# Kernel optimization log

Hardware: AMD Instinct MI355X
Metric: run time of the kernel (lower is better)

Reference implementation:

```python
import jax, jax.numpy as jnp
import numpy as np

B, T, HID = 2, 2048, 1536
H, HKV, D = 12, 2, 128
EPS = 1e-6
NEG = -1e9


def setup_inputs() -> dict:
    key = jax.random.key(0)
    ks = jax.random.split(key, 8)
    # rotary embeddings built from real angles (cos/sin of position*inv_freq)
    inv_freq = 1.0 / (10000.0 ** (jnp.arange(0, D, 2, dtype=jnp.float32) / D))  # [D/2]
    pos = jnp.arange(T, dtype=jnp.float32)
    ang = pos[:, None] * inv_freq[None, :]                       # [T, D/2]
    emb = jnp.concatenate([ang, ang], axis=-1)                   # [T, D]
    cos = jnp.broadcast_to(jnp.cos(emb)[None], (B, T, D))
    sin = jnp.broadcast_to(jnp.sin(emb)[None], (B, T, D))
    # additive causal mask [1,1,T,T]
    causal = jnp.tril(jnp.ones((T, T), dtype=bool))
    attention_mask = jnp.where(causal, 0.0, NEG).astype(jnp.float32)[None, None]
    s = 0.02
    return {
        "hidden_states": jax.random.normal(ks[0], (B, T, HID), jnp.float32),
        "cos": cos,
        "sin": sin,
        "attention_mask": attention_mask,
        "q_w": jax.random.normal(ks[1], (H * D, HID), jnp.float32) * s,
        "k_w": jax.random.normal(ks[2], (HKV * D, HID), jnp.float32) * s,
        "v_w": jax.random.normal(ks[3], (HKV * D, HID), jnp.float32) * s,
        "o_w": jax.random.normal(ks[4], (HID, H * D), jnp.float32) * s,
        "q_norm_w": jnp.ones((D,), jnp.float32),
        "k_norm_w": jnp.ones((D,), jnp.float32),
    }


def _rms_norm(x, w):
    # per-head RMSNorm over last dim (head_dim), computed in fp32
    xf = x.astype(jnp.float32)
    var = jnp.mean(xf * xf, axis=-1, keepdims=True)
    return (w * (xf * jax.lax.rsqrt(var + EPS))).astype(x.dtype)


def _rotate_half(x):
    x1, x2 = jnp.split(x, 2, axis=-1)
    return jnp.concatenate([-x2, x1], axis=-1)


def reference(hidden_states, cos, sin, attention_mask, q_w, k_w, v_w, o_w, q_norm_w, k_norm_w):
    b, t, _ = hidden_states.shape
    n_rep = H // HKV
    scale = D ** -0.5

    # projections -> [B, n_heads, T, D]
    q = (hidden_states @ q_w.T).reshape(b, t, H, D)
    k = (hidden_states @ k_w.T).reshape(b, t, HKV, D)
    v = (hidden_states @ v_w.T).reshape(b, t, HKV, D).transpose(0, 2, 1, 3)

    # per-head QK RMSNorm, then to [B, H, T, D]
    q = _rms_norm(q, q_norm_w).transpose(0, 2, 1, 3)
    k = _rms_norm(k, k_norm_w).transpose(0, 2, 1, 3)

    # RoPE (cos/sin broadcast over head axis)
    c = cos[:, None, :, :]
    s = sin[:, None, :, :]
    q = q * c + _rotate_half(q) * s
    k = k * c + _rotate_half(k) * s

    # GQA repeat_kv: [B, HKV, T, D] -> [B, H, T, D]
    k = jnp.repeat(k, n_rep, axis=1)
    v = jnp.repeat(v, n_rep, axis=1)

    attn = jnp.einsum('bhqd,bhkd->bhqk', q, k) * scale + attention_mask
    attn = jax.nn.softmax(attn.astype(jnp.float32), axis=-1).astype(q.dtype)
    out = jnp.einsum('bhqk,bhkd->bhqd', attn, v)
    out = out.transpose(0, 2, 1, 3).reshape(b, t, H * D)
    return out @ o_w.T
```

## Files before the change

### kernel.cpp

```cpp
#include <hip/hip_runtime.h>
#include <hip/hip_bf16.h>


#define B_   2
#define T_   2048
#define HID_ 1536
#define H_   12
#define HKV_ 2
#define D_   128
#define GQ_  (H_ / HKV_)
#define NQKV_ 2048
#define SCALE_ 0.08838834764831845f

typedef unsigned short u16;
typedef __attribute__((ext_vector_type(4))) float f32x4;
typedef __attribute__((ext_vector_type(8))) short bf16x8;
typedef __attribute__((ext_vector_type(4))) unsigned short u16x4;
typedef __attribute__((ext_vector_type(8))) unsigned short u16x8;

__device__ __forceinline__ u16 f2b(float f) {
  union { __hip_bfloat16 h; u16 u; } cv;
  cv.h = __float2bfloat16(f);
  return cv.u;
}
__device__ __forceinline__ float b2f(u16 u) {
  union { float f; unsigned i; } cv;
  cv.i = ((unsigned)u) << 16;
  return cv.f;
}

__device__ __forceinline__ void glds16(const u16* g, u16* l) {
  __builtin_amdgcn_global_load_lds((const __attribute__((address_space(1))) void*)g,
                                   (__attribute__((address_space(3))) void*)l, 16, 0, 0);
}

__global__ __launch_bounds__(256) void cvt_f32_bf16(const float* __restrict__ src,
                                                    u16* __restrict__ dst, int n4) {
  int i = blockIdx.x * 256 + threadIdx.x;
  const int stride = gridDim.x * 256;
  for (; i < n4; i += stride) {
    const float4 v = reinterpret_cast<const float4*>(src)[i];
    u16x4 o = {f2b(v.x), f2b(v.y), f2b(v.z), f2b(v.w)};
    reinterpret_cast<u16x4*>(dst)[i] = o;
  }
}

__device__ __forceinline__ void cstore(float* p, float v) { *p = v; }
__device__ __forceinline__ void cstore(u16* p, float v) { *p = f2b(v); }

template <typename CT>
__global__ __launch_bounds__(256) void gemm_bt(const u16* __restrict__ A,
                                               const u16* __restrict__ W,
                                               CT* __restrict__ C,
                                               int M, int N, int K) {
  __shared__ __align__(16) u16 As[128 * 32];
  __shared__ __align__(16) u16 Ws[128 * 32];
  const int tid  = threadIdx.x;
  const int lane = tid & 63;
  const int wid  = tid >> 6;
  const int wr = wid >> 1, wc = wid & 1;
  const int l15 = lane & 15, kg = lane >> 4;
  const int rowBase = blockIdx.y * 128;
  const int colBase = blockIdx.x * 128;

  const int srow = lane >> 2;
  const int scol = (lane & 3) << 3;
  const u16* Ab = A + (size_t)(rowBase + wid * 16 + srow) * K + scol;
  const u16* Wb = W + (size_t)(colBase + wid * 16 + srow) * K + scol;
  u16* AsW = &As[wid * 512];
  u16* WsW = &Ws[wid * 512];

  const f32x4 zero4 = {0.f, 0.f, 0.f, 0.f};
  f32x4 acc[4][4];
#pragma unroll
  for (int m = 0; m < 4; ++m)
#pragma unroll
    for (int n = 0; n < 4; ++n) acc[m][n] = zero4;

  for (int k0 = 0; k0 < K; k0 += 32) {
    __syncthreads();
    glds16(Ab + k0, AsW);
    glds16(Ab + (size_t)64 * K + k0, AsW + 2048);
    glds16(Wb + k0, WsW);
    glds16(Wb + (size_t)64 * K + k0, WsW + 2048);
    __syncthreads();
    bf16x8 a[4], b[4];
#pragma unroll
    for (int m = 0; m < 4; ++m)
      a[m] = *reinterpret_cast<const bf16x8*>(&As[(wr * 64 + m * 16 + l15) * 32 + kg * 8]);
#pragma unroll
    for (int n = 0; n < 4; ++n)
      b[n] = *reinterpret_cast<const bf16x8*>(&Ws[(wc * 64 + n * 16 + l15) * 32 + kg * 8]);
#pragma unroll
    for (int m = 0; m < 4; ++m)
#pragma unroll
      for (int n = 0; n < 4; ++n)
        acc[m][n] = __builtin_amdgcn_mfma_f32_16x16x32_bf16(a[m], b[n], acc[m][n], 0, 0, 0);
  }
#pragma unroll
  for (int m = 0; m < 4; ++m) {
    const int row0 = rowBase + wr * 64 + m * 16 + kg * 4;
#pragma unroll
    for (int n = 0; n < 4; ++n) {
      const int col = colBase + wc * 64 + n * 16 + l15;
#pragma unroll
      for (int r = 0; r < 4; ++r) cstore(&C[(size_t)(row0 + r) * N + col], acc[m][n][r]);
    }
  }
}

__global__ __launch_bounds__(256) void norm_rope_cvt(
    const u16* __restrict__ qkv, const float* __restrict__ cosb,
    const float* __restrict__ sinb, const float* __restrict__ q_nw,
    const float* __restrict__ k_nw, u16* __restrict__ q_b,
    u16* __restrict__ k_b, u16* __restrict__ vt_b) {
  const int gwave = (int)((blockIdx.x * 256 + threadIdx.x) >> 6);
  const int lane = threadIdx.x & 63;
  const int NQ = B_ * T_ * H_;
  const int NK = B_ * T_ * HKV_;
  if (gwave < NQ) {
    const int bt = gwave / H_, h = gwave - bt * H_;
    const u16* src = qkv + (size_t)bt * NQKV_ + h * D_;
    const float x1 = b2f(src[lane]), x2 = b2f(src[lane + 64]);
    float ss = x1 * x1 + x2 * x2;
#pragma unroll
    for (int m = 32; m >= 1; m >>= 1) ss += __shfl_xor(ss, m);
    const float rinv = rsqrtf(ss * (1.0f / D_) + 1e-6f);
    const float c1 = cosb[(size_t)bt * D_ + lane], c2 = cosb[(size_t)bt * D_ + lane + 64];
    const float s1 = sinb[(size_t)bt * D_ + lane], s2 = sinb[(size_t)bt * D_ + lane + 64];
    const float n1 = x1 * rinv * q_nw[lane], n2 = x2 * rinv * q_nw[lane + 64];
    const float o1 = (n1 * c1 - n2 * s1) * SCALE_;
    const float o2 = (n2 * c2 + n1 * s2) * SCALE_;
    const int b = bt >> 11, t = bt & (T_ - 1);
    u16* dst = q_b + ((size_t)(b * H_ + h) * T_ + t) * D_;
    dst[lane] = f2b(o1);
    dst[lane + 64] = f2b(o2);
  } else if (gwave < NQ + NK) {
    const int r = gwave - NQ;
    const int bt = r >> 1, hv = r & 1;
    const u16* src = qkv + (size_t)bt * NQKV_ + 1536 + hv * D_;
    const float x1 = b2f(src[lane]), x2 = b2f(src[lane + 64]);
    float ss = x1 * x1 + x2 * x2;
#pragma unroll
    for (int m = 32; m >= 1; m >>= 1) ss += __shfl_xor(ss, m);
    const float rinv = rsqrtf(ss * (1.0f / D_) + 1e-6f);
    const float c1 = cosb[(size_t)bt * D_ + lane], c2 = cosb[(size_t)bt * D_ + lane + 64];
    const float s1 = sinb[(size_t)bt * D_ + lane], s2 = sinb[(size_t)bt * D_ + lane + 64];
    const float n1 = x1 * rinv * k_nw[lane], n2 = x2 * rinv * k_nw[lane + 64];
    const float o1 = n1 * c1 - n2 * s1;
    const float o2 = n2 * c2 + n1 * s2;
    const int b = bt >> 11, t = bt & (T_ - 1);
    u16* dst = k_b + ((size_t)(b * HKV_ + hv) * T_ + t) * D_;
    dst[lane] = f2b(o1);
    dst[lane + 64] = f2b(o2);
  } else {
    const int r = gwave - NQ - NK;
    const int bt = r >> 1, hv = r & 1;
    const u16* src = qkv + (size_t)bt * NQKV_ + 1792 + hv * D_;
    const float x1 = b2f(src[lane]), x2 = b2f(src[lane + 64]);
    const int b = bt >> 11, t = bt & (T_ - 1);
    const int kk = t & 63;
    const int tp = (t & ~63) | (kk & 32) | (((kk >> 2) & 3) << 3) |
                   (((kk >> 4) & 1) << 2) | (kk & 3);
    u16* dst = vt_b + (size_t)(b * HKV_ + hv) * D_ * T_;
    dst[(size_t)lane * T_ + tp] = f2b(x1);
    dst[(size_t)(lane + 64) * T_ + tp] = f2b(x2);
  }
}

__constant__ int QT_ARR[40] = {15,15,15,15,14,14,11,11,11,10, 7, 7, 3,
                               14,14,13,13,13,13,12,12,10,10, 9, 9, 6, 6,
                               12,12, 9, 8, 8, 8, 5, 5, 2,
                                4, 4, 1, 0};
__constant__ int C_ARR[40]  = { 0, 1, 2, 3, 0, 1, 0, 1, 2, 0, 0, 1,-1,
                                2, 3, 0, 1, 2, 3, 0, 1, 1, 2, 0, 1, 0, 1,
                                2, 3, 2, 0, 1, 2, 0, 1,-1,
                                0, 1,-1,-1};
__device__ __forceinline__ int nc_of(int qt) { return (qt < 8) ? 2 : ((qt < 12) ? 3 : 4); }
__device__ __forceinline__ int mlbase_of(int qt) {
  return (qt < 8) ? 2 * (qt - 4) : ((qt < 12) ? 8 + 3 * (qt - 8) : 20 + 4 * (qt - 12));
}
__device__ __forceinline__ int pbase_of(int qt) {
  return (qt < 8) ? (qt - 4) : ((qt < 12) ? 4 + 2 * (qt - 8) : 12 + 3 * (qt - 12));
}

__global__ __launch_bounds__(256) void attn_kernel(const u16* __restrict__ q_b,
                                                   const u16* __restrict__ k_b,
                                                   const u16* __restrict__ vt_b,
                                                   u16* __restrict__ aout,
                                                   u16* __restrict__ po0,
                                                   float2* __restrict__ ml) {
  __shared__ __align__(16) u16 Ks[64 * 128];
  __shared__ __align__(16) u16 Vs[128 * 64];
  const int id = blockIdx.x;
  const int item = id / 24;
  const int bh = id - item * 24;
  const int qt = QT_ARR[item];
  const int c = C_ARR[item];
  int kt0, ktend;
  bool partial;
  if (c < 0) {
    kt0 = 0; ktend = 2 * qt + 1; partial = false;
  } else {
    const int nt = 2 * qt + 2;
    const int nc = nc_of(qt);
    const int base = nt / nc, rem = nt - base * nc;
    kt0 = c * base + (c < rem ? c : rem);
    ktend = kt0 + base + (c < rem ? 1 : 0) - 1;
    partial = true;
  }
  const int b = bh / H_, h = bh - b * H_;
  const int kvh = h / GQ_;
  const int tid = threadIdx.x;
  const int w = tid >> 6, lane = tid & 63;
  const int l15 = lane & 15, kg = lane >> 4;
  const int qbase = qt * 128;

  const u16* Kb = k_b + (size_t)(b * HKV_ + kvh) * T_ * D_;
  const u16* Vb = vt_b + (size_t)(b * HKV_ + kvh) * D_ * T_;

  bf16x8 qf[2][4];
#pragma unroll
  for (int qb = 0; qb < 2; ++qb) {
    const u16* qrow =
        q_b + ((size_t)(b * H_ + h) * T_ + qbase + w * 32 + qb * 16 + l15) * D_;
#pragma unroll
    for (int s4 = 0; s4 < 4; ++s4)
      qf[qb][s4] = *reinterpret_cast<const bf16x8*>(qrow + s4 * 32 + kg * 8);
  }

  int kK[4], vK[4];
#pragma unroll
  for (int cc = 0; cc < 4; ++cc) {
    const int ch = w * 4 + cc;
    const int kr = ch * 4 + (lane >> 4);
    kK[cc] = kr * D_ + (((lane & 15) << 3) ^ ((kr & 7) << 3));
    const int dr = ch * 8 + (lane >> 3);
    vK[cc] = dr * T_ + (((lane & 7) << 3) ^ ((dr & 7) << 3));
  }

  const int xorv = (l15 & 7) << 3;

  const f32x4 zero4 = {0.f, 0.f, 0.f, 0.f};
  f32x4 o[2][8];
#pragma unroll
  for (int qb = 0; qb < 2; ++qb)
#pragma unroll
    for (int n = 0; n < 8; ++n) o[qb][n] = zero4;
  float m[2] = {0.f, 0.f};
  float lsum[2] = {0.f, 0.f};

  for (int kt = kt0; kt <= ktend; ++kt) {
    __syncthreads();
    {
      const size_t kb = (size_t)kt * 64;
#pragma unroll
      for (int cc = 0; cc < 4; ++cc) {
        glds16(Kb + kb * D_ + kK[cc], &Ks[(w * 4 + cc) * 512]);
        glds16(Vb + kb + vK[cc], &Vs[(w * 4 + cc) * 512]);
      }
    }
    __syncthreads();
    f32x4 sc[2][4];
#pragma unroll
    for (int qb = 0; qb < 2; ++qb)
#pragma unroll
      for (int n = 0; n < 4; ++n) sc[qb][n] = zero4;
    __builtin_amdgcn_s_setprio(1);
#pragma unroll
    for (int n = 0; n < 4; ++n)
#pragma unroll
      for (int s4 = 0; s4 < 4; ++s4) {
        const int koff = (n * 16 + l15) * 128 + ((s4 * 32 + kg * 8) ^ xorv);
        bf16x8 kf = *reinterpret_cast<const bf16x8*>(&Ks[koff]);
#pragma unroll
        for (int qb = 0; qb < 2; ++qb)
          sc[qb][n] = __builtin_amdgcn_mfma_f32_16x16x32_bf16(kf, qf[qb][s4],
                                                              sc[qb][n], 0, 0, 0);
      }
    __builtin_amdgcn_s_setprio(0);
    if (kt >= 2 * qt) {
#pragma unroll
      for (int qb = 0; qb < 2; ++qb) {
        const int qg = w * 32 + qb * 16 + l15;
        const int kbb = (kt - 2 * qt) * 64;
#pragma unroll
        for (int n = 0; n < 4; ++n)
#pragma unroll
          for (int r = 0; r < 4; ++r)
            if (kbb + n * 16 + kg * 4 + r > qg) sc[qb][n][r] = -3e38f;
      }
    }
    float pm[2];
#pragma unroll
    for (int qb = 0; qb < 2; ++qb) {
      float v = sc[qb][0][0];
#pragma unroll
      for (int n = 0; n < 4; ++n)
#pragma unroll
        for (int r = 0; r < 4; ++r) v = fmaxf(v, sc[qb][n][r]);
      v = fmaxf(v, __shfl_xor(v, 16));
      v = fmaxf(v, __shfl_xor(v, 32));
      pm[qb] = v;
    }
    if (__any((pm[0] > m[0] + 8.f) | (pm[1] > m[1] + 8.f))) {
#pragma unroll
      for (int qb = 0; qb < 2; ++qb) {
        const float mn = fmaxf(m[qb], pm[qb]);
        const float al = __expf(m[qb] - mn);
        m[qb] = mn;
        lsum[qb] *= al;
        float alT[4];
#pragma unroll
        for (int r = 0; r < 4; ++r)
          alT[r] = __shfl(al, (lane & 48) | (kg * 4 + r));
#pragma unroll
        for (int n = 0; n < 8; ++n)
#pragma unroll
          for (int r = 0; r < 4; ++r) o[qb][n][r] *= alT[r];
      }
    }
#pragma unroll
    for (int qb = 0; qb < 2; ++qb) {
      float rs = 0.f;
#pragma unroll
      for (int n = 0; n < 4; ++n)
#pragma unroll
        for (int r = 0; r < 4; ++r) {
          const float p = __expf(sc[qb][n][r] - m[qb]);
          sc[qb][n][r] = p;
          rs += p;
        }
      rs += __shfl_xor(rs, 16);
      rs += __shfl_xor(rs, 32);
      lsum[qb] += rs;
    }
    bf16x8 pf[2][2];
#pragma unroll
    for (int qb = 0; qb < 2; ++qb)
#pragma unroll
      for (int ks = 0; ks < 2; ++ks)
#pragma unroll
        for (int r = 0; r < 4; ++r) {
          pf[qb][ks][r] = (short)f2b(sc[qb][2 * ks][r]);
          pf[qb][ks][r + 4] = (short)f2b(sc[qb][2 * ks + 1][r]);
        }
    __builtin_amdgcn_s_setprio(1);
#pragma unroll
    for (int n = 0; n < 8; ++n)
#pragma unroll
      for (int ks = 0; ks < 2; ++ks) {
        const int voff = (n * 16 + l15) * 64 + ((ks * 32 + kg * 8) ^ xorv);
        bf16x8 vf = *reinterpret_cast<const bf16x8*>(&Vs[voff]);
#pragma unroll
        for (int qb = 0; qb < 2; ++qb)
          o[qb][n] = __builtin_amdgcn_mfma_f32_16x16x32_bf16(pf[qb][ks], vf,
                                                             o[qb][n], 0, 0, 0);
      }
    __builtin_amdgcn_s_setprio(0);
  }

  if (!partial) {
    float invT[2][4];
#pragma unroll
    for (int qb = 0; qb < 2; ++qb) {
      const float inv = 1.0f / lsum[qb];
#pragma unroll
      for (int r = 0; r < 4; ++r)
        invT[qb][r] = __shfl(inv, (lane & 48) | (kg * 4 + r));
    }
#pragma unroll
    for (int qb = 0; qb < 2; ++qb) {
      const int t0 = qbase + w * 32 + qb * 16 + kg * 4;
#pragma unroll
      for (int n = 0; n < 8; ++n)
#pragma unroll
        for (int r = 0; r < 4; ++r)
          aout[(size_t)(b * T_ + t0 + r) * (H_ * D_) + h * D_ + n * 16 + l15] =
              f2b(o[qb][n][r] * invT[qb][r]);
    }
  } else {
    const int mlslot = bh * 36 + mlbase_of(qt) + c;
    if (kg == 0) {
#pragma unroll
      for (int qb = 0; qb < 2; ++qb) {
        float2 v;
        v.x = m[qb];
        v.y = lsum[qb];
        ml[(size_t)mlslot * 128 + w * 32 + qb * 16 + l15] = v;
      }
    }
    if (c == 0) {
#pragma unroll
      for (int qb = 0; qb < 2; ++qb) {
        const int t0 = qbase + w * 32 + qb * 16 + kg * 4;
#pragma unroll
        for (int n = 0; n < 8; ++n)
#pragma unroll
          for (int r = 0; r < 4; ++r)
            aout[(size_t)(b * T_ + t0 + r) * (H_ * D_) + h * D_ + n * 16 + l15] =
                f2b(o[qb][n][r]);
      }
    } else {
      const int pslot = bh * 24 + pbase_of(qt) + (c - 1);
#pragma unroll
      for (int qb = 0; qb < 2; ++qb) {
        const int row0 = w * 32 + qb * 16 + kg * 4;
#pragma unroll
        for (int n = 0; n < 8; ++n)
#pragma unroll
          for (int r = 0; r < 4; ++r)
            po0[((size_t)pslot * 128 + row0 + r) * 128 + n * 16 + l15] =
                f2b(o[qb][n][r]);
      }
    }
  }
}

__global__ __launch_bounds__(256) void combine_kernel(u16* __restrict__ aout,
                                                      const u16* __restrict__ po0,
                                                      const float2* __restrict__ ml) {
  const int qt = 4 + blockIdx.x;
  const int bh = blockIdx.y;
  const int nc = nc_of(qt);
  const int mlb = bh * 36 + mlbase_of(qt);
  const int pb = bh * 24 + pbase_of(qt);
  const int b = bh / H_, h = bh - b * H_;
  const int t0 = qt * 128;
  const int tid = threadIdx.x;
  const int row = tid >> 1;
  const int colc = (tid & 1) << 6;

  float ms[4], ls[4];
  float mm = -3e38f;
  for (int cc = 0; cc < nc; ++cc) {
    const float2 v = ml[(size_t)(mlb + cc) * 128 + row];
    ms[cc] = v.x; ls[cc] = v.y;
    mm = fmaxf(mm, v.x);
  }
  float lt = 0.f;
  float scl[4];
  for (int cc = 0; cc < nc; ++cc) {
    scl[cc] = __expf(ms[cc] - mm);
    lt += ls[cc] * scl[cc];
  }
  const float inv = 1.0f / lt;
  for (int cc = 0; cc < nc; ++cc) scl[cc] *= inv;

  u16* a = aout + (size_t)(b * T_ + t0 + row) * (H_ * D_) + h * D_ + colc;
#pragma unroll
  for (int j = 0; j < 8; ++j) {
    u16x8 v0 = *reinterpret_cast<const u16x8*>(a + j * 8);
    float acc[8];
#pragma unroll
    for (int e = 0; e < 8; ++e) acc[e] = b2f(v0[e]) * scl[0];
    for (int cc = 1; cc < nc; ++cc) {
      const u16* p = po0 + ((size_t)(pb + cc - 1) * 128 + row) * 128 + colc;
      u16x8 vc = *reinterpret_cast<const u16x8*>(p + j * 8);
#pragma unroll
      for (int e = 0; e < 8; ++e) acc[e] += b2f(vc[e]) * scl[cc];
    }
    u16x8 outv;
#pragma unroll
    for (int e = 0; e < 8; ++e) outv[e] = f2b(acc[e]);
    *reinterpret_cast<u16x8*>(a + j * 8) = outv;
  }
}

extern "C" void kernel_launch(void* const* d_in, const int* in_sizes, int n_in,
                              void* d_out, int out_size, void* d_ws, size_t ws_size,
                              hipStream_t stream) {
  const float* hidden = (const float*)d_in[0];
  const float* cosb   = (const float*)d_in[1];
  const float* sinb   = (const float*)d_in[2];
  const float* q_w  = (const float*)d_in[4];
  const float* k_w  = (const float*)d_in[5];
  const float* v_w  = (const float*)d_in[6];
  const float* o_w  = (const float*)d_in[7];
  const float* q_nw = (const float*)d_in[8];
  const float* k_nw = (const float*)d_in[9];
  float* out = (float*)d_out;

  char* ws = (char*)d_ws;
  const size_t MB = 1u << 20;
  u16*    hidden_b = (u16*)(ws);
  u16*    qkvw     = (u16*)(ws + 12 * MB);
  u16*    q_b      = (u16*)(ws);
  u16*    aout     = (u16*)(ws + 12 * MB);
  float2* ml       = (float2*)(ws + 24 * MB);
  u16*    k_b      = (u16*)(ws + 25 * MB);
  u16*    vt_b     = (u16*)(ws + 27 * MB);
  u16*    owb      = (u16*)(ws + 29 * MB);
  u16*    qkv_proj = (u16*)d_out;
  u16*    po0      = (u16*)d_out;

  const dim3 blk(256);
  const int M = B_ * T_;

  {
    const int nh = (B_ * T_ * HID_) / 4;
    const int nq = (H_ * D_ * HID_) / 4;
    const int nk = (HKV_ * D_ * HID_) / 4;
    cvt_f32_bf16<<<2048, blk, 0, stream>>>(hidden, hidden_b, nh);
    cvt_f32_bf16<<<2048, blk, 0, stream>>>(q_w, qkvw, nq);
    cvt_f32_bf16<<<384, blk, 0, stream>>>(k_w, qkvw + (size_t)1536 * HID_, nk);
    cvt_f32_bf16<<<384, blk, 0, stream>>>(v_w, qkvw + (size_t)1792 * HID_, nk);
    cvt_f32_bf16<<<2048, blk, 0, stream>>>(o_w, owb, nq);
  }

  gemm_bt<u16><<<dim3(NQKV_ / 128, M / 128), blk, 0, stream>>>(hidden_b, qkvw, qkv_proj,
                                                               M, NQKV_, HID_);

  norm_rope_cvt<<<16384, blk, 0, stream>>>(qkv_proj, cosb, sinb, q_nw, k_nw,
                                           q_b, k_b, vt_b);

  attn_kernel<<<960, blk, 0, stream>>>(q_b, k_b, vt_b, aout, po0, ml);
  combine_kernel<<<dim3(12, B_ * H_), blk, 0, stream>>>(aout, po0, ml);

  gemm_bt<float><<<dim3(HID_ / 128, M / 128), blk, 0, stream>>>(aout, owb, out,
                                                                M, HID_, HID_);
}
```

Before: 211.0 us.

## Fuse QK norm, RoPE and V transpose into QKV GEMM epilogue; use exp2 softmax

The QKV projection GEMM now stages its output tile in shared memory and applies per-head RMSNorm, RoPE and scaling directly in the epilogue, writing q/k/vt in the attention layout. This removes the separate norm_rope kernel and the round trip of the intermediate qkv buffer through global memory. The GEMM K-step is widened from 32 to 64, the three weight conversions are merged into one launch, and the log2(e) factor is folded into the Q scale so the softmax uses exp2f. The cost is a larger shared-memory footprint and a serial per-row epilogue loop within each block.

```diff
diff --git a/kernel.cpp b/kernel.cpp
--- a/kernel.cpp
+++ b/kernel.cpp
@@ -10,7 +10,8 @@
 #define D_   128
 #define GQ_  (H_ / HKV_)
 #define NQKV_ 2048
-#define SCALE_ 0.08838834764831845f
+#define LOG2E_ 1.4426950408889634f
+#define SCALE2_ (0.08838834764831845f * LOG2E_)
 
 typedef unsigned short u16;
 typedef __attribute__((ext_vector_type(4))) float f32x4;
@@ -45,16 +46,31 @@
   }
 }
 
-__device__ __forceinline__ void cstore(float* p, float v) { *p = v; }
-__device__ __forceinline__ void cstore(u16* p, float v) { *p = f2b(v); }
-
-template <typename CT>
+#define NQ4_ 589824
+#define NK4_ 98304
+__global__ __launch_bounds__(256) void cvt_wqkv(const float* __restrict__ q_w,
+                                                const float* __restrict__ k_w,
+                                                const float* __restrict__ v_w,
+                                                u16* __restrict__ qkvw) {
+  int i = blockIdx.x * 256 + threadIdx.x;
+  const int stride = gridDim.x * 256;
+  const int total = NQ4_ + 2 * NK4_;
+  for (; i < total; i += stride) {
+    float4 v;
+    if (i < NQ4_) v = reinterpret_cast<const float4*>(q_w)[i];
+    else if (i < NQ4_ + NK4_) v = reinterpret_cast<const float4*>(k_w)[i - NQ4_];
+    else v = reinterpret_cast<const float4*>(v_w)[i - NQ4_ - NK4_];
+    u16x4 o = {f2b(v.x), f2b(v.y), f2b(v.z), f2b(v.w)};
+    reinterpret_cast<u16x4*>(qkvw)[i] = o;
+  }
+}
+
 __global__ __launch_bounds__(256) void gemm_bt(const u16* __restrict__ A,
                                                const u16* __restrict__ W,
-                                               CT* __restrict__ C,
+                                               float* __restrict__ C,
                                                int M, int N, int K) {
-  __shared__ __align__(16) u16 As[128 * 32];
-  __shared__ __align__(16) u16 Ws[128 * 32];
+  __shared__ __align__(16) u16 As[128 * 64];
+  __shared__ __align__(16) u16 Ws[128 * 64];
   const int tid  = threadIdx.x;
   const int lane = tid & 63;
   const int wid  = tid >> 6;
@@ -63,12 +79,10 @@
   const int rowBase = blockIdx.y * 128;
   const int colBase = blockIdx.x * 128;
 
-  const int srow = lane >> 2;
-  const int scol = (lane & 3) << 3;
-  const u16* Ab = A + (size_t)(rowBase + wid * 16 + srow) * K + scol;
-  const u16* Wb = W + (size_t)(colBase + wid * 16 + srow) * K + scol;
-  u16* AsW = &As[wid * 512];
-  u16* WsW = &Ws[wid * 512];
+  const int srow = lane >> 3;
+  const int scol = (lane & 7) << 3;
+  const u16* Ab = A + (size_t)(rowBase + wid * 32 + srow) * K + scol;
+  const u16* Wb = W + (size_t)(colBase + wid * 32 + srow) * K + scol;
 
   const f32x4 zero4 = {0.f, 0.f, 0.f, 0.f};
   f32x4 acc[4][4];
@@ -77,25 +91,35 @@
 #pragma unroll
     for (int n = 0; n < 4; ++n) acc[m][n] = zero4;
 
-  for (int k0 = 0; k0 < K; k0 += 32) {
+  for (int k0 = 0; k0 < K; k0 += 64) {
     __syncthreads();
-    glds16(Ab + k0, AsW);
-    glds16(Ab + (size_t)64 * K + k0, AsW + 2048);
-    glds16(Wb + k0, WsW);
-    glds16(Wb + (size_t)64 * K + k0, WsW + 2048);
+#pragma unroll
+    for (int c = 0; c < 4; ++c) {
+      glds16(Ab + (size_t)(c * 8) * K + k0, &As[(wid * 4 + c) * 512]);
+      glds16(Wb + (size_t)(c * 8) * K + k0, &Ws[(wid * 4 + c) * 512]);
+    }
     __syncthreads();
-    bf16x8 a[4], b[4];
+    bf16x8 a[4][2], b[4][2];
 #pragma unroll
     for (int m = 0; m < 4; ++m)
-      a[m] = *reinterpret_cast<const bf16x8*>(&As[(wr * 64 + m * 16 + l15) * 32 + kg * 8]);
+#pragma unroll
+      for (int ks = 0; ks < 2; ++ks)
+        a[m][ks] = *reinterpret_cast<const bf16x8*>(
+            &As[(wr * 64 + m * 16 + l15) * 64 + ks * 32 + kg * 8]);
 #pragma unroll
     for (int n = 0; n < 4; ++n)
-      b[n] = *reinterpret_cast<const bf16x8*>(&Ws[(wc * 64 + n * 16 + l15) * 32 + kg * 8]);
+#pragma unroll
+      for (int ks = 0; ks < 2; ++ks)
+        b[n][ks] = *reinterpret_cast<const bf16x8*>(
+            &Ws[(wc * 64 + n * 16 + l15) * 64 + ks * 32 + kg * 8]);
 #pragma unroll
     for (int m = 0; m < 4; ++m)
 #pragma unroll
       for (int n = 0; n < 4; ++n)
-        acc[m][n] = __builtin_amdgcn_mfma_f32_16x16x32_bf16(a[m], b[n], acc[m][n], 0, 0, 0);
+#pragma unroll
+        for (int ks = 0; ks < 2; ++ks)
+          acc[m][n] = __builtin_amdgcn_mfma_f32_16x16x32_bf16(a[m][ks], b[n][ks],
+                                                              acc[m][n], 0, 0, 0);
   }
 #pragma unroll
   for (int m = 0; m < 4; ++m) {
@@ -104,67 +128,120 @@
     for (int n = 0; n < 4; ++n) {
       const int col = colBase + wc * 64 + n * 16 + l15;
 #pragma unroll
-      for (int r = 0; r < 4; ++r) cstore(&C[(size_t)(row0 + r) * N + col], acc[m][n][r]);
-    }
-  }
-}
-
-__global__ __launch_bounds__(256) void norm_rope_cvt(
-    const u16* __restrict__ qkv, const float* __restrict__ cosb,
-    const float* __restrict__ sinb, const float* __restrict__ q_nw,
-    const float* __restrict__ k_nw, u16* __restrict__ q_b,
-    u16* __restrict__ k_b, u16* __restrict__ vt_b) {
-  const int gwave = (int)((blockIdx.x * 256 + threadIdx.x) >> 6);
-  const int lane = threadIdx.x & 63;
-  const int NQ = B_ * T_ * H_;
-  const int NK = B_ * T_ * HKV_;
-  if (gwave < NQ) {
-    const int bt = gwave / H_, h = gwave - bt * H_;
-    const u16* src = qkv + (size_t)bt * NQKV_ + h * D_;
-    const float x1 = b2f(src[lane]), x2 = b2f(src[lane + 64]);
-    float ss = x1 * x1 + x2 * x2;
-#pragma unroll
-    for (int m = 32; m >= 1; m >>= 1) ss += __shfl_xor(ss, m);
-    const float rinv = rsqrtf(ss * (1.0f / D_) + 1e-6f);
-    const float c1 = cosb[(size_t)bt * D_ + lane], c2 = cosb[(size_t)bt * D_ + lane + 64];
-    const float s1 = sinb[(size_t)bt * D_ + lane], s2 = sinb[(size_t)bt * D_ + lane + 64];
-    const float n1 = x1 * rinv * q_nw[lane], n2 = x2 * rinv * q_nw[lane + 64];
-    const float o1 = (n1 * c1 - n2 * s1) * SCALE_;
-    const float o2 = (n2 * c2 + n1 * s2) * SCALE_;
-    const int b = bt >> 11, t = bt & (T_ - 1);
-    u16* dst = q_b + ((size_t)(b * H_ + h) * T_ + t) * D_;
-    dst[lane] = f2b(o1);
-    dst[lane + 64] = f2b(o2);
-  } else if (gwave < NQ + NK) {
-    const int r = gwave - NQ;
-    const int bt = r >> 1, hv = r & 1;
-    const u16* src = qkv + (size_t)bt * NQKV_ + 1536 + hv * D_;
-    const float x1 = b2f(src[lane]), x2 = b2f(src[lane + 64]);
-    float ss = x1 * x1 + x2 * x2;
-#pragma unroll
-    for (int m = 32; m >= 1; m >>= 1) ss += __shfl_xor(ss, m);
-    const float rinv = rsqrtf(ss * (1.0f / D_) + 1e-6f);
-    const float c1 = cosb[(size_t)bt * D_ + lane], c2 = cosb[(size_t)bt * D_ + lane + 64];
-    const float s1 = sinb[(size_t)bt * D_ + lane], s2 = sinb[(size_t)bt * D_ + lane + 64];
-    const float n1 = x1 * rinv * k_nw[lane], n2 = x2 * rinv * k_nw[lane + 64];
-    const float o1 = n1 * c1 - n2 * s1;
-    const float o2 = n2 * c2 + n1 * s2;
-    const int b = bt >> 11, t = bt & (T_ - 1);
-    u16* dst = k_b + ((size_t)(b * HKV_ + hv) * T_ + t) * D_;
-    dst[lane] = f2b(o1);
-    dst[lane + 64] = f2b(o2);
+      for (int r = 0; r < 4; ++r) C[(size_t)(row0 + r) * N + col] = acc[m][n][r];
+    }
+  }
+}
+
+__global__ __launch_bounds__(256) void gemm_qkv(
+    const u16* __restrict__ A, const u16* __restrict__ W,
+    const float* __restrict__ cosb, const float* __restrict__ sinb,
+    const float* __restrict__ q_nw, const float* __restrict__ k_nw,
+    u16* __restrict__ q_b, u16* __restrict__ k_b, u16* __restrict__ vt_b) {
+  __shared__ __align__(16) u16 smem[128 * 137];
+  u16* As = smem;
+  u16* Ws = smem + 8192;
+  const int tid  = threadIdx.x;
+  const int lane = tid & 63;
+  const int wid  = tid >> 6;
+  const int wr = wid >> 1, wc = wid & 1;
+  const int l15 = lane & 15, kg = lane >> 4;
+  const int rowBase = blockIdx.y * 128;
+  const int colBase = blockIdx.x * 128;
+  const int K = HID_;
+
+  const int srow = lane >> 3;
+  const int scol = (lane & 7) << 3;
+  const u16* Ab = A + (size_t)(rowBase + wid * 32 + srow) * K + scol;
+  const u16* Wb = W + (size_t)(colBase + wid * 32 + srow) * K + scol;
+
+  const f32x4 zero4 = {0.f, 0.f, 0.f, 0.f};
+  f32x4 acc[4][4];
+#pragma unroll
+  for (int m = 0; m < 4; ++m)
+#pragma unroll
+    for (int n = 0; n < 4; ++n) acc[m][n] = zero4;
+
+  for (int k0 = 0; k0 < K; k0 += 64) {
+    __syncthreads();
+#pragma unroll
+    for (int c = 0; c < 4; ++c) {
+      glds16(Ab + (size_t)(c * 8) * K + k0, &As[(wid * 4 + c) * 512]);
+      glds16(Wb + (size_t)(c * 8) * K + k0, &Ws[(wid * 4 + c) * 512]);
+    }
+    __syncthreads();
+    bf16x8 a[4][2], b[4][2];
+#pragma unroll
+    for (int m = 0; m < 4; ++m)
+#pragma unroll
+      for (int ks = 0; ks < 2; ++ks)
+        a[m][ks] = *reinterpret_cast<const bf16x8*>(
+            &As[(wr * 64 + m * 16 + l15) * 64 + ks * 32 + kg * 8]);
+#pragma unroll
+    for (int n = 0; n < 4; ++n)
+#pragma unroll
+      for (int ks = 0; ks < 2; ++ks)
+        b[n][ks] = *reinterpret_cast<const bf16x8*>(
+            &Ws[(wc * 64 + n * 16 + l15) * 64 + ks * 32 + kg * 8]);
+#pragma unroll
+    for (int m = 0; m < 4; ++m)
+#pragma unroll
+      for (int n = 0; n < 4; ++n)
+#pragma unroll
+        for (int ks = 0; ks < 2; ++ks)
+          acc[m][n] = __builtin_amdgcn_mfma_f32_16x16x32_bf16(a[m][ks], b[n][ks],
+                                                              acc[m][n], 0, 0, 0);
+  }
+
+  __syncthreads();
+#pragma unroll
+  for (int m = 0; m < 4; ++m)
+#pragma unroll
+    for (int n = 0; n < 4; ++n)
+#pragma unroll
+      for (int r = 0; r < 4; ++r)
+        smem[(wr * 64 + m * 16 + kg * 4 + r) * 137 + wc * 64 + n * 16 + l15] =
+            f2b(acc[m][n][r]);
+  __syncthreads();
+
+  const int ct = blockIdx.x;
+  const int b = rowBase >> 11;
+  if (ct < 14) {
+    const float* nw = (ct < 12) ? q_nw : k_nw;
+    const float nwl = nw[lane], nwh = nw[lane + 64];
+    const float sc = (ct < 12) ? SCALE2_ : 1.0f;
+    u16* dstbase = (ct < 12) ? (q_b + (size_t)(b * H_ + ct) * T_ * D_)
+                             : (k_b + (size_t)(b * HKV_ + (ct - 12)) * T_ * D_);
+    for (int i = 0; i < 32; ++i) {
+      const int row = wid * 32 + i;
+      const int tok = rowBase + row;
+      const int t = tok & (T_ - 1);
+      const float x1 = b2f(smem[row * 137 + lane]);
+      const float x2 = b2f(smem[row * 137 + lane + 64]);
+      float ss = x1 * x1 + x2 * x2;
+#pragma unroll
+      for (int msk = 32; msk >= 1; msk >>= 1) ss += __shfl_xor(ss, msk);
+      const float rinv = rsqrtf(ss * (1.0f / D_) + 1e-6f);
+      const float c1 = cosb[(size_t)tok * D_ + lane];
+      const float c2 = cosb[(size_t)tok * D_ + lane + 64];
+      const float s1 = sinb[(size_t)tok * D_ + lane];
+      const float s2 = sinb[(size_t)tok * D_ + lane + 64];
+      const float n1 = x1 * rinv * nwl, n2 = x2 * rinv * nwh;
+      u16* dst = dstbase + (size_t)t * D_;
+      dst[lane] = f2b((n1 * c1 - n2 * s1) * sc);
+      dst[lane + 64] = f2b((n2 * c2 + n1 * s2) * sc);
+    }
   } else {
-    const int r = gwave - NQ - NK;
-    const int bt = r >> 1, hv = r & 1;
-    const u16* src = qkv + (size_t)bt * NQKV_ + 1792 + hv * D_;
-    const float x1 = b2f(src[lane]), x2 = b2f(src[lane + 64]);
-    const int b = bt >> 11, t = bt & (T_ - 1);
-    const int kk = t & 63;
-    const int tp = (t & ~63) | (kk & 32) | (((kk >> 2) & 3) << 3) |
-                   (((kk >> 4) & 1) << 2) | (kk & 3);
-    u16* dst = vt_b + (size_t)(b * HKV_ + hv) * D_ * T_;
-    dst[(size_t)lane * T_ + tp] = f2b(x1);
-    dst[(size_t)(lane + 64) * T_ + tp] = f2b(x2);
+    const int hv = ct - 14;
+    const int tp = (lane & 32) | (((lane >> 2) & 3) << 3) | (((lane >> 4) & 1) << 2) |
+                   (lane & 3);
+    u16* vb = vt_b + (size_t)(b * HKV_ + hv) * D_ * T_;
+    const int tb = rowBase & (T_ - 1);
+    for (int it = 0; it < 64; ++it) {
+      const int d = wid * 32 + (it >> 1), half = it & 1;
+      const float x = b2f(smem[(half * 64 + lane) * 137 + d]);
+      vb[(size_t)d * T_ + tb + half * 64 + tp] = f2b(x);
+    }
   }
 }
 
@@ -238,7 +315,6 @@
     const int dr = ch * 8 + (lane >> 3);
     vK[cc] = dr * T_ + (((lane & 7) << 3) ^ ((dr & 7) << 3));
   }
-
   const int xorv = (l15 & 7) << 3;
 
   const f32x4 zero4 = {0.f, 0.f, 0.f, 0.f};
@@ -307,7 +383,7 @@
 #pragma unroll
       for (int qb = 0; qb < 2; ++qb) {
         const float mn = fmaxf(m[qb], pm[qb]);
-        const float al = __expf(m[qb] - mn);
+        const float al = exp2f(m[qb] - mn);
         m[qb] = mn;
         lsum[qb] *= al;
         float alT[4];
@@ -327,7 +403,7 @@
       for (int n = 0; n < 4; ++n)
 #pragma unroll
         for (int r = 0; r < 4; ++r) {
-          const float p = __expf(sc[qb][n][r] - m[qb]);
+          const float p = exp2f(sc[qb][n][r] - m[qb]);
           sc[qb][n][r] = p;
           rs += p;
         }
@@ -441,7 +517,7 @@
   float lt = 0.f;
   float scl[4];
   for (int cc = 0; cc < nc; ++cc) {
-    scl[cc] = __expf(ms[cc] - mm);
+    scl[cc] = exp2f(ms[cc] - mm);
     lt += ls[cc] * scl[cc];
   }
   const float inv = 1.0f / lt;
@@ -485,38 +561,28 @@
   const size_t MB = 1u << 20;
   u16*    hidden_b = (u16*)(ws);
   u16*    qkvw     = (u16*)(ws + 12 * MB);
-  u16*    q_b      = (u16*)(ws);
-  u16*    aout     = (u16*)(ws + 12 * MB);
-  float2* ml       = (float2*)(ws + 24 * MB);
-  u16*    k_b      = (u16*)(ws + 25 * MB);
-  u16*    vt_b     = (u16*)(ws + 27 * MB);
-  u16*    owb      = (u16*)(ws + 29 * MB);
-  u16*    qkv_proj = (u16*)d_out;
+  u16*    q_b      = (u16*)(ws + 18 * MB);
+  u16*    k_b      = (u16*)(ws + 30 * MB);
+  u16*    vt_b     = (u16*)(ws + 32 * MB);
+  u16*    aout     = (u16*)(ws);
+  u16*    owb      = (u16*)(ws + 12 * MB);
+  float2* ml       = (float2*)(ws + 17 * MB);
   u16*    po0      = (u16*)d_out;
 
   const dim3 blk(256);
   const int M = B_ * T_;
 
-  {
-    const int nh = (B_ * T_ * HID_) / 4;
-    const int nq = (H_ * D_ * HID_) / 4;
-    const int nk = (HKV_ * D_ * HID_) / 4;
-    cvt_f32_bf16<<<2048, blk, 0, stream>>>(hidden, hidden_b, nh);
-    cvt_f32_bf16<<<2048, blk, 0, stream>>>(q_w, qkvw, nq);
-    cvt_f32_bf16<<<384, blk, 0, stream>>>(k_w, qkvw + (size_t)1536 * HID_, nk);
-    cvt_f32_bf16<<<384, blk, 0, stream>>>(v_w, qkvw + (size_t)1792 * HID_, nk);
-    cvt_f32_bf16<<<2048, blk, 0, stream>>>(o_w, owb, nq);
-  }
-
-  gemm_bt<u16><<<dim3(NQKV_ / 128, M / 128), blk, 0, stream>>>(hidden_b, qkvw, qkv_proj,
-                                                               M, NQKV_, HID_);
-
-  norm_rope_cvt<<<16384, blk, 0, stream>>>(qkv_proj, cosb, sinb, q_nw, k_nw,
-                                           q_b, k_b, vt_b);
+  cvt_f32_bf16<<<2048, blk, 0, stream>>>(hidden, hidden_b, (B_ * T_ * HID_) / 4);
+  cvt_wqkv<<<3072, blk, 0, stream>>>(q_w, k_w, v_w, qkvw);
+
+  gemm_qkv<<<dim3(NQKV_ / 128, M / 128), blk, 0, stream>>>(
+      hidden_b, qkvw, cosb, sinb, q_nw, k_nw, q_b, k_b, vt_b);
+
+  cvt_f32_bf16<<<2048, blk, 0, stream>>>(o_w, owb, (H_ * D_ * HID_) / 4);
 
   attn_kernel<<<960, blk, 0, stream>>>(q_b, k_b, vt_b, aout, po0, ml);
   combine_kernel<<<dim3(12, B_ * H_), blk, 0, stream>>>(aout, po0, ml);
 
-  gemm_bt<float><<<dim3(HID_ / 128, M / 128), blk, 0, stream>>>(aout, owb, out,
-                                                                M, HID_, HID_);
-}
+  gemm_bt<<<dim3(HID_ / 128, M / 128), blk, 0, stream>>>(aout, owb, out,
+                                                         M, HID_, HID_);
+}
```

New measurement: 203.1 us. 1.04x faster.
